# Kernel optimization log

Measured on AMD Instinct MI355X. Metric: run time of the kernel, lower is better.

The kernel has to match this reference:

```python
import jax, jax.numpy as jnp
import numpy as np


def setup_inputs() -> dict:
    key = jax.random.key(0)
    k1, k2, k3, k4, k5, k6 = jax.random.split(key, 6)
    NODE, TAG, E, D, B = 100000, 10000, 4, 32, 524288
    INIT = 0.001
    return {
        "tag_table": INIT * jax.random.normal(k1, (TAG, D), dtype=jnp.float32),
        "node_tables": INIT * jax.random.normal(k2, (E, NODE, D), dtype=jnp.float32),
        "activate": jnp.zeros((NODE, E), dtype=jnp.float32),
        "pos_node": jax.random.randint(k3, (B,), 0, NODE),
        "pos_tag": jax.random.randint(k4, (B,), 0, TAG),
        "neg_node": jax.random.randint(k5, (B,), 0, NODE),
        "neg_tag": jax.random.randint(k6, (B,), 0, TAG),
    }


def _node_tag_dist(node_tables, tag_table, node_list, tag_list):
    # tag_emb: [B, D]; per-table node emb: [E, B, D]
    tag_emb = tag_table[tag_list]
    node_emb = node_tables[:, node_list, :]  # [E, B, D]
    # eu_dist = -sum(x*y, dim=1) for each table -> [B, E]
    dists = -jnp.einsum("ebd,bd->be", node_emb, tag_emb)
    min_idx = jnp.argmin(dists, axis=1)          # [B]
    dist = jnp.min(dists, axis=1, keepdims=True)  # [B, 1]
    return dist, min_idx


def reference(tag_table, node_tables, activate, pos_node, pos_tag, neg_node, neg_tag):
    # positive branch (pos=True): update activate counter with argmin choices
    pos_dist, pos_idx = _node_tag_dist(node_tables, tag_table, pos_node, pos_tag)
    activate_new = activate.at[pos_node, pos_idx].add(1.0)
    pos_loss = -jnp.sum(jax.nn.log_sigmoid(-pos_dist))
    # negative branch (no counter update)
    neg_dist, _ = _node_tag_dist(node_tables, tag_table, neg_node, neg_tag)
    neg_loss = -jnp.sum(jax.nn.log_sigmoid(neg_dist))
    loss = pos_loss + neg_loss
    return loss, activate_new
```

## Files before the change

### kernel.cpp

```cpp
#include <hip/hip_runtime.h>

#define NODES 100000
#define NTAG  10000
#define NE    4
#define ND    32
#define NB    524288

constexpr int TPB   = 512;
constexpr int BNODE = 32;
constexpr int NBUCK = NODES / BNODE;
constexpr int CAP   = 512;
constexpr int MBLK  = 1024;

constexpr int STPB  = 1024;
constexpr int CHUNK = 8192;
constexpr int SBLK  = 2 * NB / CHUNK;

constexpr size_t OFF_REC = 16384;
constexpr size_t WS_NEED = OFF_REC + (size_t)NBUCK * CAP * 4;

__device__ __forceinline__ void gload_lds16(const void* g, void* l) {
    __builtin_amdgcn_global_load_lds(
        (const __attribute__((address_space(1))) unsigned int*)g,
        (__attribute__((address_space(3))) unsigned int*)l, 16, 0, 0);
}
__device__ __forceinline__ void gload_lds4(const void* g, void* l) {
    __builtin_amdgcn_global_load_lds(
        (const __attribute__((address_space(1))) unsigned int*)g,
        (__attribute__((address_space(3))) unsigned int*)l, 4, 0, 0);
}

template <int CTRL>
__device__ __forceinline__ double bfly_dpp(double v) {
    const int lo = __builtin_amdgcn_update_dpp(0, __double2loint(v), CTRL, 0xF, 0xF, true);
    const int hi = __builtin_amdgcn_update_dpp(0, __double2hiint(v), CTRL, 0xF, 0xF, true);
    return __hiloint2double(hi, lo);
}
__device__ __forceinline__ double bfly_swz4(double v) {
    const int lo = __builtin_amdgcn_ds_swizzle(__double2loint(v), 0x101F);
    const int hi = __builtin_amdgcn_ds_swizzle(__double2hiint(v), 0x101F);
    return __hiloint2double(hi, lo);
}
template <int CTRL>
__device__ __forceinline__ float bflyf_dpp(float v) {
    return __int_as_float(__builtin_amdgcn_update_dpp(0, __float_as_int(v), CTRL, 0xF, 0xF, true));
}
__device__ __forceinline__ float bflyf_swz4(float v) {
    return __int_as_float(__builtin_amdgcn_ds_swizzle(__float_as_int(v), 0x101F));
}


__global__ __launch_bounds__(256) void init_kernel(float* __restrict__ out,
                                                   int* __restrict__ cnt) {
    const int i = blockIdx.x * 256 + threadIdx.x;
    if (i < NBUCK)  cnt[i] = 0;
    if (i == NBUCK) out[0] = 0.f;
}

__global__ __launch_bounds__(STPB) void scatter_kernel(
    const int* __restrict__ pos_node, const int* __restrict__ pos_tag,
    const int* __restrict__ neg_node, const int* __restrict__ neg_tag,
    int* __restrict__ cnt_g, uint32_t* __restrict__ rec)
{
    __shared__ uint32_t lrec[CHUNK];
    __shared__ int lcnt[NBUCK];
    __shared__ int lbase[NBUCK];

    const int tid = threadIdx.x;
    const int blk = blockIdx.x;
    const bool is_pos = blk < (SBLK / 2);
    const int  base = (is_pos ? blk : blk - SBLK / 2) * CHUNK;
    const int* __restrict__ nsrc = is_pos ? pos_node : neg_node;
    const int* __restrict__ tsrc = is_pos ? pos_tag  : neg_tag;

    for (int i = tid; i < NBUCK; i += STPB) lcnt[i] = 0;
    __syncthreads();

    #pragma unroll
    for (int r = 0; r < CHUNK / STPB; ++r) {
        const int i = r * STPB + tid;
        const int node = nsrc[base + i];
        const int tag  = tsrc[base + i];
        lrec[i] = ((uint32_t)node << 15) | ((uint32_t)tag << 1) | (is_pos ? 1u : 0u);
        atomicAdd(&lcnt[node >> 5], 1);
    }
    __syncthreads();

    for (int i = tid; i < NBUCK; i += STPB) {
        const int c = lcnt[i];
        lbase[i] = c ? atomicAdd(&cnt_g[i], c) : 0;
        lcnt[i]  = 0;
    }
    __syncthreads();

    #pragma unroll
    for (int r = 0; r < CHUNK / STPB; ++r) {
        const int i = r * STPB + tid;
        const uint32_t v = lrec[i];
        const int bk = (int)(v >> 20);
        const int p  = lbase[bk] + atomicAdd(&lcnt[bk], 1);
        if (p < CAP)
            rec[(size_t)bk * CAP + p] = v;
    }
}

__global__ __launch_bounds__(TPB, 8) void main_kernel(
    const float* __restrict__ tag_table, const float* __restrict__ node_tables,
    const float* __restrict__ act,
    const int* __restrict__ cnt_g, const uint32_t* __restrict__ rec,
    float* __restrict__ out)
{
    __shared__ float    nlds[2][NE * BNODE * ND];
    __shared__ uint32_t recs_s[2][CAP];
    __shared__ uint32_t hist[BNODE * NE];
    __shared__ float sm[TPB / 64];

    const int tid  = threadIdx.x;
    const int g    = tid & 7;
    const int grp  = tid >> 3;
    const int wave = tid >> 6;
    const uint32_t goff = (uint32_t)g << 4;

    const char* tagb = (const char*)tag_table;
    const float4* __restrict__ nsrc4 = (const float4*)node_tables;

    const int nb = 1 + (NBUCK - 1 - blockIdx.x) / MBLK;

    auto stage = [&](int b, int bk) {
        const uint32_t nbase = (uint32_t)bk * BNODE;
        #pragma unroll
        for (int r = 0; r < 2; ++r) {
            const int f = r * TPB + tid;
            const float4* gs = &nsrc4[(size_t)(f >> 8) * (NODES * 8)
                                      + (size_t)nbase * 8 + (f & 255)];
            char* ld = (char*)nlds[b] + (size_t)(r * TPB + wave * 64) * 16;
            gload_lds16(gs, ld);
        }
        const uint32_t* rg = rec + (size_t)bk * CAP;
        char* ld = (char*)recs_s[b] + (size_t)wave * 256;
        gload_lds4(rg + tid, ld);
    };

    if (tid < BNODE * NE) hist[tid] = 0;

    int n_cur = min(cnt_g[blockIdx.x], CAP);
    stage(0, blockIdx.x);
    __syncthreads();

    float local = 0.f;
    int cur = 0;

    for (int ib = 0; ib < nb; ++ib) {
        const int bk = blockIdx.x + ib * MBLK;
        const int n  = n_cur;
        const uint32_t nbase = (uint32_t)bk * BNODE;

        const bool have_nxt = (ib + 1 < nb);
        if (have_nxt) {
            const int bkn = bk + MBLK;
            stage(cur ^ 1, bkn);
            n_cur = min(cnt_g[bkn], CAP);
        }

        const float*    bufc = nlds[cur];
        const uint32_t* recc = recs_s[cur];
        for (int j = grp; j < n; j += TPB / 8) {
            const uint32_t rr = recc[j];
            const uint32_t node = rr >> 15, tag = (rr >> 1) & 0x3FFFu;
            const int lr = (int)(node & 31u);

            const float4 cc = *(const float4*)(tagb + ((tag << 7) + goff));
            const float* rp = bufc + (lr << 5) + (g << 2);
            const float4 a0 = *(const float4*)(rp);
            const float4 a1 = *(const float4*)(rp + 1024);
            const float4 a2 = *(const float4*)(rp + 2048);
            const float4 a3 = *(const float4*)(rp + 3072);

            float q0 = fmaf(a0.w, cc.w, fmaf(a0.z, cc.z, fmaf(a0.y, cc.y, a0.x * cc.x)));
            float q1 = fmaf(a1.w, cc.w, fmaf(a1.z, cc.z, fmaf(a1.y, cc.y, a1.x * cc.x)));
            float q2 = fmaf(a2.w, cc.w, fmaf(a2.z, cc.z, fmaf(a2.y, cc.y, a2.x * cc.x)));
            float q3 = fmaf(a3.w, cc.w, fmaf(a3.z, cc.z, fmaf(a3.y, cc.y, a3.x * cc.x)));

            q0 += bflyf_dpp<0xB1>(q0); q1 += bflyf_dpp<0xB1>(q1);
            q2 += bflyf_dpp<0xB1>(q2); q3 += bflyf_dpp<0xB1>(q3);
            q0 += bflyf_dpp<0x4E>(q0); q1 += bflyf_dpp<0x4E>(q1);
            q2 += bflyf_dpp<0x4E>(q2); q3 += bflyf_dpp<0x4E>(q3);
            q0 += bflyf_swz4(q0); q1 += bflyf_swz4(q1);
            q2 += bflyf_swz4(q2); q3 += bflyf_swz4(q3);

            float m1 = q0; int idx = 0;
            if (q1 > m1) { m1 = q1; idx = 1; }
            if (q2 > m1) { m1 = q2; idx = 2; }
            if (q3 > m1) { m1 = q3; idx = 3; }
            const float h01 = fmaxf(q0, q1), l01 = fminf(q0, q1);
            const float h23 = fmaxf(q2, q3), l23 = fminf(q2, q3);
            const float m2 = fmaxf(fminf(h01, h23), (h01 > h23) ? l01 : l23);

            float best = m1;
            if (m1 - m2 < 1e-7f) {
                const double tx = (double)cc.x, ty = (double)cc.y, tz = (double)cc.z, tw = (double)cc.w;
                double d0 = (double)a0.x*tx + (double)a0.y*ty + (double)a0.z*tz + (double)a0.w*tw;
                double d1 = (double)a1.x*tx + (double)a1.y*ty + (double)a1.z*tz + (double)a1.w*tw;
                double d2 = (double)a2.x*tx + (double)a2.y*ty + (double)a2.z*tz + (double)a2.w*tw;
                double d3 = (double)a3.x*tx + (double)a3.y*ty + (double)a3.z*tz + (double)a3.w*tw;
                d0 += bfly_dpp<0xB1>(d0); d1 += bfly_dpp<0xB1>(d1);
                d2 += bfly_dpp<0xB1>(d2); d3 += bfly_dpp<0xB1>(d3);
                d0 += bfly_dpp<0x4E>(d0); d1 += bfly_dpp<0x4E>(d1);
                d2 += bfly_dpp<0x4E>(d2); d3 += bfly_dpp<0x4E>(d3);
                d0 += bfly_swz4(d0); d1 += bfly_swz4(d1);
                d2 += bfly_swz4(d2); d3 += bfly_swz4(d3);
                double b = d0; idx = 0;
                if (d1 > b) { b = d1; idx = 1; }
                if (d2 > b) { b = d2; idx = 2; }
                if (d3 > b) { b = d3; idx = 3; }
                best = (float)b;
            }

            const bool  pos = (rr & 1u);
            const float x   = pos ? -best : best;
            const float e   = __expf(-fabsf(x));
            local += fmaxf(x, 0.f) + __logf(1.f + e);

            if (pos && g == 0)
                atomicAdd(&hist[(node & 31u) * NE + idx], 1u);
        }

        __syncthreads();

        if (tid < BNODE * NE) {
            const uint32_t cell = nbase * NE + tid;
            out[1 + cell] = act[cell] + (float)hist[tid];
            hist[tid] = 0;
        }
        __syncthreads();
        cur ^= 1;
    }

    #pragma unroll
    for (int off = 1; off < 64; off <<= 1) local += __shfl_xor(local, off, 64);
    if ((tid & 63) == 0) sm[tid >> 6] = local;
    __syncthreads();
    if (tid == 0) {
        float tot = 0.f;
        #pragma unroll
        for (int w = 0; w < TPB / 64; ++w) tot += sm[w];
        atomicAdd(out, tot * 0.125f);
    }
}


__global__ __launch_bounds__(256) void fb_init(const float* __restrict__ act,
                                               float* __restrict__ out,
                                               double* __restrict__ ws, int npart) {
    int i = blockIdx.x * 256 + threadIdx.x;
    if (i < NODES * NE) out[1 + i] = act[i];
    if (i < npart)      ws[i] = 0.0;
}

__global__ __launch_bounds__(256) void fb_main(
    const float* __restrict__ tag_table, const float* __restrict__ node_tables,
    const int* __restrict__ pos_node, const int* __restrict__ pos_tag,
    const int* __restrict__ neg_node, const int* __restrict__ neg_tag,
    float* __restrict__ out, double* __restrict__ ws, int npart)
{
    const int tid = threadIdx.x;
    const int g   = tid & 7;
    const int grp = tid >> 3;
    const uint32_t goff = (uint32_t)g << 4;
    const int total = 2 * NB;
    constexpr int FNB = 2048, FGRP = FNB * 32;

    const char* tagb  = (const char*)tag_table;
    const char* nodb0 = (const char*)node_tables;
    const char* nodb1 = nodb0 + (size_t)NODES * 128;
    const char* nodb2 = nodb1 + (size_t)NODES * 128;
    const char* nodb3 = nodb2 + (size_t)NODES * 128;

    float local = 0.f;
    for (int s = blockIdx.x * 32 + grp; s < total; s += FGRP) {
        const bool is_pos = s < NB;
        const int  b    = is_pos ? s : s - NB;
        const int  node = is_pos ? pos_node[b] : neg_node[b];
        const int  tag  = is_pos ? pos_tag[b]  : neg_tag[b];
        const uint32_t no = ((uint32_t)node << 7) + goff, to = ((uint32_t)tag << 7) + goff;
        const float4 t  = *(const float4*)(tagb  + to);
        const float4 n0 = *(const float4*)(nodb0 + no);
        const float4 n1 = *(const float4*)(nodb1 + no);
        const float4 n2 = *(const float4*)(nodb2 + no);
        const float4 n3 = *(const float4*)(nodb3 + no);
        const double tx = (double)t.x, ty = (double)t.y, tz = (double)t.z, tw = (double)t.w;
        double q0 = (double)n0.x*tx + (double)n0.y*ty + (double)n0.z*tz + (double)n0.w*tw;
        double q1 = (double)n1.x*tx + (double)n1.y*ty + (double)n1.z*tz + (double)n1.w*tw;
        double q2 = (double)n2.x*tx + (double)n2.y*ty + (double)n2.z*tz + (double)n2.w*tw;
        double q3 = (double)n3.x*tx + (double)n3.y*ty + (double)n3.z*tz + (double)n3.w*tw;
        #pragma unroll
        for (int off = 1; off < 8; off <<= 1) {
            q0 += __shfl_xor(q0, off, 64); q1 += __shfl_xor(q1, off, 64);
            q2 += __shfl_xor(q2, off, 64); q3 += __shfl_xor(q3, off, 64);
        }
        double best = q0; int idx = 0;
        if (q1 > best) { best = q1; idx = 1; }
        if (q2 > best) { best = q2; idx = 2; }
        if (q3 > best) { best = q3; idx = 3; }
        const float x = is_pos ? (float)(-best) : (float)best;
        const float e = __expf(-fabsf(x));
        local += fmaxf(x, 0.f) + __logf(1.f + e);
        if (is_pos && g == 0) atomicAdd(out + 1 + ((size_t)node << 2) + idx, 1.0f);
    }
    #pragma unroll
    for (int off = 1; off < 64; off <<= 1) local += __shfl_xor(local, off, 64);
    __shared__ double sm[4];
    if ((tid & 63) == 0) sm[tid >> 6] = (double)local;
    __syncthreads();
    if (tid == 0) {
        double tot = 0.0;
        #pragma unroll
        for (int w = 0; w < 4; ++w) tot += sm[w];
        atomicAdd(&ws[blockIdx.x & (npart - 1)], tot * 0.125);
    }
}

__global__ __launch_bounds__(256) void fb_final(const double* __restrict__ loss_part,
                                                float* __restrict__ out, int npart) {
    __shared__ double sm[256];
    double v = 0.0;
    for (int i = threadIdx.x; i < npart; i += 256) v += loss_part[i];
    sm[threadIdx.x] = v;
    __syncthreads();
    for (int s = 128; s > 0; s >>= 1) {
        if (threadIdx.x < s) sm[threadIdx.x] += sm[threadIdx.x + s];
        __syncthreads();
    }
    if (threadIdx.x == 0) out[0] = (float)sm[0];
}


extern "C" void kernel_launch(void* const* d_in, const int* in_sizes, int n_in,
                              void* d_out, int out_size, void* d_ws, size_t ws_size,
                              hipStream_t stream) {
    const float* tag_table   = (const float*)d_in[0];
    const float* node_tables = (const float*)d_in[1];
    const float* activate    = (const float*)d_in[2];
    const int*   pos_node    = (const int*)d_in[3];
    const int*   pos_tag     = (const int*)d_in[4];
    const int*   neg_node    = (const int*)d_in[5];
    const int*   neg_tag     = (const int*)d_in[6];
    float* out = (float*)d_out;

    if (ws_size >= WS_NEED) {
        int*      cnt = (int*)d_ws;
        uint32_t* rec = (uint32_t*)((char*)d_ws + OFF_REC);

        hipLaunchKernelGGL(init_kernel, dim3((NBUCK + 256) / 256 + 1), dim3(256), 0, stream,
                           out, cnt);
        hipLaunchKernelGGL(scatter_kernel, dim3(SBLK), dim3(STPB), 0, stream,
                           pos_node, pos_tag, neg_node, neg_tag, cnt, rec);
        hipLaunchKernelGGL(main_kernel, dim3(MBLK), dim3(TPB), 0, stream,
                           tag_table, node_tables, activate, cnt, rec, out);
    } else {
        double* ws = (double*)d_ws;
        int npart = 1;
        while (npart * 2 <= 2048 && (size_t)(npart * 2) * sizeof(double) <= ws_size) npart *= 2;
        const int init_blocks = (NODES * NE + 255) / 256;
        hipLaunchKernelGGL(fb_init, dim3(init_blocks), dim3(256), 0, stream,
                           activate, out, ws, npart);
        hipLaunchKernelGGL(fb_main, dim3(2048), dim3(256), 0, stream,
                           tag_table, node_tables, pos_node, pos_tag, neg_node, neg_tag,
                           out, ws, npart);
        hipLaunchKernelGGL(fb_final, dim3(1), dim3(256), 0, stream, ws, out, npart);
    }
}
```

Baseline: 57.54 us.

## Use 33-node buckets so every block handles at most three buckets

Bucket width grows from 32 to 33 nodes, so there are fewer buckets (3031 instead of 3125) and no block of the 1024-block main grid gets a fourth bucket. This removes the tail iteration that only some blocks ran. Staging, indexing and histogram code now use a general bucket width with bounds checks for the last partial bucket. The last step of the 8-lane reduction uses DPP row_half_mirror instead of ds_swizzle. The costs are integer divisions in the scatter pass and slightly more records per bucket against the fixed 512 capacity.

```diff
diff --git a/kernel.cpp b/kernel.cpp
--- a/kernel.cpp
+++ b/kernel.cpp
@@ -7,8 +7,8 @@
 #define NB    524288
 
 constexpr int TPB   = 512;
-constexpr int BNODE = 32;
-constexpr int NBUCK = NODES / BNODE;
+constexpr int BNODE = 33;
+constexpr int NBUCK = (NODES + BNODE - 1) / BNODE;
 constexpr int CAP   = 512;
 constexpr int MBLK  = 1024;
 
@@ -18,6 +18,9 @@
 
 constexpr size_t OFF_REC = 16384;
 constexpr size_t WS_NEED = OFF_REC + (size_t)NBUCK * CAP * 4;
+
+constexpr int PL_F4  = BNODE * 8;
+constexpr int TOT_F4 = NE * PL_F4;
 
 __device__ __forceinline__ void gload_lds16(const void* g, void* l) {
     __builtin_amdgcn_global_load_lds(
@@ -36,17 +39,9 @@
     const int hi = __builtin_amdgcn_update_dpp(0, __double2hiint(v), CTRL, 0xF, 0xF, true);
     return __hiloint2double(hi, lo);
 }
-__device__ __forceinline__ double bfly_swz4(double v) {
-    const int lo = __builtin_amdgcn_ds_swizzle(__double2loint(v), 0x101F);
-    const int hi = __builtin_amdgcn_ds_swizzle(__double2hiint(v), 0x101F);
-    return __hiloint2double(hi, lo);
-}
 template <int CTRL>
 __device__ __forceinline__ float bflyf_dpp(float v) {
     return __int_as_float(__builtin_amdgcn_update_dpp(0, __float_as_int(v), CTRL, 0xF, 0xF, true));
-}
-__device__ __forceinline__ float bflyf_swz4(float v) {
-    return __int_as_float(__builtin_amdgcn_ds_swizzle(__float_as_int(v), 0x101F));
 }
 
 
@@ -82,7 +77,7 @@
         const int node = nsrc[base + i];
         const int tag  = tsrc[base + i];
         lrec[i] = ((uint32_t)node << 15) | ((uint32_t)tag << 1) | (is_pos ? 1u : 0u);
-        atomicAdd(&lcnt[node >> 5], 1);
+        atomicAdd(&lcnt[node / BNODE], 1);
     }
     __syncthreads();
 
@@ -97,7 +92,7 @@
     for (int r = 0; r < CHUNK / STPB; ++r) {
         const int i = r * STPB + tid;
         const uint32_t v = lrec[i];
-        const int bk = (int)(v >> 20);
+        const int bk = (int)(v >> 15) / BNODE;
         const int p  = lbase[bk] + atomicAdd(&lcnt[bk], 1);
         if (p < CAP)
             rec[(size_t)bk * CAP + p] = v;
@@ -129,12 +124,17 @@
     auto stage = [&](int b, int bk) {
         const uint32_t nbase = (uint32_t)bk * BNODE;
         #pragma unroll
-        for (int r = 0; r < 2; ++r) {
+        for (int r = 0; r < 3; ++r) {
             const int f = r * TPB + tid;
-            const float4* gs = &nsrc4[(size_t)(f >> 8) * (NODES * 8)
-                                      + (size_t)nbase * 8 + (f & 255)];
-            char* ld = (char*)nlds[b] + (size_t)(r * TPB + wave * 64) * 16;
-            gload_lds16(gs, ld);
+            const int p   = f / PL_F4;
+            const int rem = f - p * PL_F4;
+            const int row = rem >> 3;
+            if (f < TOT_F4 && nbase + row < NODES) {
+                const float4* gs = &nsrc4[(size_t)p * (NODES * 8)
+                                          + ((size_t)nbase + row) * 8 + (rem & 7)];
+                char* ld = (char*)nlds[b] + (size_t)(r * TPB + wave * 64) * 16;
+                gload_lds16(gs, ld);
+            }
         }
         const uint32_t* rg = rec + (size_t)bk * CAP;
         char* ld = (char*)recs_s[b] + (size_t)wave * 256;
@@ -167,26 +167,26 @@
         for (int j = grp; j < n; j += TPB / 8) {
             const uint32_t rr = recc[j];
             const uint32_t node = rr >> 15, tag = (rr >> 1) & 0x3FFFu;
-            const int lr = (int)(node & 31u);
+            const uint32_t lr = node - nbase;
 
             const float4 cc = *(const float4*)(tagb + ((tag << 7) + goff));
             const float* rp = bufc + (lr << 5) + (g << 2);
             const float4 a0 = *(const float4*)(rp);
-            const float4 a1 = *(const float4*)(rp + 1024);
-            const float4 a2 = *(const float4*)(rp + 2048);
-            const float4 a3 = *(const float4*)(rp + 3072);
+            const float4 a1 = *(const float4*)(rp + PL_F4 * 4);
+            const float4 a2 = *(const float4*)(rp + PL_F4 * 8);
+            const float4 a3 = *(const float4*)(rp + PL_F4 * 12);
 
             float q0 = fmaf(a0.w, cc.w, fmaf(a0.z, cc.z, fmaf(a0.y, cc.y, a0.x * cc.x)));
             float q1 = fmaf(a1.w, cc.w, fmaf(a1.z, cc.z, fmaf(a1.y, cc.y, a1.x * cc.x)));
             float q2 = fmaf(a2.w, cc.w, fmaf(a2.z, cc.z, fmaf(a2.y, cc.y, a2.x * cc.x)));
             float q3 = fmaf(a3.w, cc.w, fmaf(a3.z, cc.z, fmaf(a3.y, cc.y, a3.x * cc.x)));
 
-            q0 += bflyf_dpp<0xB1>(q0); q1 += bflyf_dpp<0xB1>(q1);
-            q2 += bflyf_dpp<0xB1>(q2); q3 += bflyf_dpp<0xB1>(q3);
-            q0 += bflyf_dpp<0x4E>(q0); q1 += bflyf_dpp<0x4E>(q1);
-            q2 += bflyf_dpp<0x4E>(q2); q3 += bflyf_dpp<0x4E>(q3);
-            q0 += bflyf_swz4(q0); q1 += bflyf_swz4(q1);
-            q2 += bflyf_swz4(q2); q3 += bflyf_swz4(q3);
+            q0 += bflyf_dpp<0xB1>(q0);  q1 += bflyf_dpp<0xB1>(q1);
+            q2 += bflyf_dpp<0xB1>(q2);  q3 += bflyf_dpp<0xB1>(q3);
+            q0 += bflyf_dpp<0x4E>(q0);  q1 += bflyf_dpp<0x4E>(q1);
+            q2 += bflyf_dpp<0x4E>(q2);  q3 += bflyf_dpp<0x4E>(q3);
+            q0 += bflyf_dpp<0x141>(q0); q1 += bflyf_dpp<0x141>(q1);
+            q2 += bflyf_dpp<0x141>(q2); q3 += bflyf_dpp<0x141>(q3);
 
             float m1 = q0; int idx = 0;
             if (q1 > m1) { m1 = q1; idx = 1; }
@@ -203,12 +203,12 @@
                 double d1 = (double)a1.x*tx + (double)a1.y*ty + (double)a1.z*tz + (double)a1.w*tw;
                 double d2 = (double)a2.x*tx + (double)a2.y*ty + (double)a2.z*tz + (double)a2.w*tw;
                 double d3 = (double)a3.x*tx + (double)a3.y*ty + (double)a3.z*tz + (double)a3.w*tw;
-                d0 += bfly_dpp<0xB1>(d0); d1 += bfly_dpp<0xB1>(d1);
-                d2 += bfly_dpp<0xB1>(d2); d3 += bfly_dpp<0xB1>(d3);
-                d0 += bfly_dpp<0x4E>(d0); d1 += bfly_dpp<0x4E>(d1);
-                d2 += bfly_dpp<0x4E>(d2); d3 += bfly_dpp<0x4E>(d3);
-                d0 += bfly_swz4(d0); d1 += bfly_swz4(d1);
-                d2 += bfly_swz4(d2); d3 += bfly_swz4(d3);
+                d0 += bfly_dpp<0xB1>(d0);  d1 += bfly_dpp<0xB1>(d1);
+                d2 += bfly_dpp<0xB1>(d2);  d3 += bfly_dpp<0xB1>(d3);
+                d0 += bfly_dpp<0x4E>(d0);  d1 += bfly_dpp<0x4E>(d1);
+                d2 += bfly_dpp<0x4E>(d2);  d3 += bfly_dpp<0x4E>(d3);
+                d0 += bfly_dpp<0x141>(d0); d1 += bfly_dpp<0x141>(d1);
+                d2 += bfly_dpp<0x141>(d2); d3 += bfly_dpp<0x141>(d3);
                 double b = d0; idx = 0;
                 if (d1 > b) { b = d1; idx = 1; }
                 if (d2 > b) { b = d2; idx = 2; }
@@ -222,14 +222,14 @@
             local += fmaxf(x, 0.f) + __logf(1.f + e);
 
             if (pos && g == 0)
-                atomicAdd(&hist[(node & 31u) * NE + idx], 1u);
+                atomicAdd(&hist[lr * NE + idx], 1u);
         }
 
         __syncthreads();
 
         if (tid < BNODE * NE) {
             const uint32_t cell = nbase * NE + tid;
-            out[1 + cell] = act[cell] + (float)hist[tid];
+            if (cell < NODES * NE) out[1 + cell] = act[cell] + (float)hist[tid];
             hist[tid] = 0;
         }
         __syncthreads();
```

After: 58.88 us. 2.3% more time.
